# Performance work log

Hardware: AMD Instinct MI355X
Metric: run time of the kernel (lower is better)

The kernel has to match this reference:

```python
import jax, jax.numpy as jnp
import numpy as np

D = 1024      # model dim
DH = 64       # dim_head
H = 8         # heads
INNER = DH * H
L = 6         # depth
NL = 64       # num_latents
MF = 128      # max_num_frames
FF = 4 * D    # ff_mult * dim
B, T, F, V = 4, 8, 4, 256


def _ln(x, g, b):
    m = x.mean(-1, keepdims=True)
    v = x.var(-1, keepdims=True)
    return (x - m) / jnp.sqrt(v + 1e-5) * g + b


def setup_inputs() -> dict:
    key = jax.random.key(0)
    ks = jax.random.split(key, 8)
    s = 0.02
    x = jax.random.normal(ks[0], (B, T, F, V, D), jnp.float32)
    latents = jax.random.normal(ks[1], (NL, D), jnp.float32)
    frame_embs = jax.random.normal(ks[2], (MF, D), jnp.float32)
    Wq = jax.random.normal(ks[3], (L, D, INNER), jnp.float32) * s
    Wkv = jax.random.normal(ks[4], (L, D, 2 * INNER), jnp.float32) * s
    Wo = jax.random.normal(ks[5], (L, INNER, D), jnp.float32) * s
    W1 = jax.random.normal(ks[6], (L, D, FF), jnp.float32) * s
    W2 = jax.random.normal(ks[7], (L, FF, D), jnp.float32) * s
    ones = jnp.ones((L, D), jnp.float32)
    zeros = jnp.zeros((L, D), jnp.float32)
    return dict(
        x=x, latents=latents, frame_embs=frame_embs,
        g_media=ones, b_media=zeros, g_lat=ones, b_lat=zeros,
        Wq=Wq, Wkv=Wkv, Wo=Wo, g_ff=ones, b_ff=zeros, W1=W1, W2=W2,
        g_out=jnp.ones((D,), jnp.float32), b_out=jnp.zeros((D,), jnp.float32),
    )


def reference(x, latents, frame_embs, g_media, b_media, g_lat, b_lat,
              Wq, Wkv, Wo, g_ff, b_ff, W1, W2, g_out, b_out):
    scale = DH ** -0.5
    # add frame embeddings (indexed by T, as in original code), merge F,v dims
    x = x + frame_embs[:T][None, :, None, None, :]
    x = x.reshape(B, T, F * V, D)
    lat0 = jnp.broadcast_to(latents, (B, T, NL, D))

    def split_heads(a):  # (b, t, n, h*d) -> (b, h, t, n, d)
        return a.reshape(B, T, -1, H, DH).transpose(0, 3, 1, 2, 4)

    def block(lat, p):
        gm, bm, gl, bl, wq, wkv, wo, gf, bf, w1, w2 = p
        xm = _ln(x, gm, bm)
        ln_l = _ln(lat, gl, bl)
        q = (ln_l @ wq) * scale
        kv = jnp.concatenate([xm, ln_l], axis=-2) @ wkv
        k, v = jnp.split(kv, 2, axis=-1)
        q, k, v = split_heads(q), split_heads(k), split_heads(v)
        sim = jnp.einsum('bhtid,bhtjd->bhtij', q, k)
        attn = jax.nn.softmax(sim, axis=-1)
        o = jnp.einsum('bhtij,bhtjd->bhtid', attn, v)
        o = o.transpose(0, 2, 3, 1, 4).reshape(B, T, NL, INNER)
        lat = o @ wo + lat
        ff = jax.nn.gelu(_ln(lat, gf, bf) @ w1, approximate=False) @ w2
        return lat + ff, None

    lat, _ = jax.lax.scan(block, lat0,
                          (g_media, b_media, g_lat, b_lat, Wq, Wkv, Wo,
                           g_ff, b_ff, W1, W2))
    return _ln(lat, g_out, b_out)
```

## Files before the change

### kernel.cpp

```cpp
#include <hip/hip_runtime.h>
#include <math.h>

#define D_      1024
#define DH_     64
#define H_      8
#define INNER_  512
#define L_      6
#define NL_     64
#define FF_     4096
#define B_      4
#define T_      8
#define FV_     1024
#define BT_     32
#define MROWS_  32768
#define NKV_    1088
#define KVROWS_ 34816
#define ZB_     256

typedef __bf16 bf16;
typedef __bf16 bf16x8 __attribute__((ext_vector_type(8)));
typedef __bf16 bf16x4 __attribute__((ext_vector_type(4)));
typedef float  f32x4  __attribute__((ext_vector_type(4)));

#define BARRIER() { asm volatile("" ::: "memory"); __builtin_amdgcn_s_barrier(); asm volatile("" ::: "memory"); }
#define ENDPH() { __builtin_amdgcn_sched_barrier(0); asm volatile("s_waitcnt lgkmcnt(0)"); __builtin_amdgcn_sched_barrier(0); BARRIER(); }

__device__ __forceinline__ void gload_lds16(const bf16* g, bf16* l) {
    __builtin_amdgcn_global_load_lds(
        (const __attribute__((address_space(1))) unsigned int*)g,
        (__attribute__((address_space(3))) unsigned int*)l, 16, 0, 0);
}

__device__ __forceinline__ float wred_sum(float v) {
#pragma unroll
    for (int o = 32; o > 0; o >>= 1) v += __shfl_xor(v, o, 64);
    return v;
}

__device__ __forceinline__ float gelu_f(float x) {
    return 0.5f * x * (1.0f + erff(x * 0.70710678118654752440f));
}

__global__ __launch_bounds__(256) void xhat_k(const float* __restrict__ x,
                                              const float* __restrict__ fe,
                                              bf16* __restrict__ xhat) {
    __shared__ float red[8];
    int row = blockIdx.x;
    int t = (row >> 10) & 7;
    const float* xr = x + (size_t)row * D_;
    const float* fr_ = fe + (size_t)t * D_;
    int tid = threadIdx.x, c = tid * 4;
    float4 v = *(const float4*)(xr + c);
    float4 f = *(const float4*)(fr_ + c);
    v.x += f.x; v.y += f.y; v.z += f.z; v.w += f.w;
    float s = v.x + v.y + v.z + v.w;
    float ss = v.x * v.x + v.y * v.y + v.z * v.z + v.w * v.w;
    s = wred_sum(s); ss = wred_sum(ss);
    if ((tid & 63) == 0) { red[tid >> 6] = s; red[4 + (tid >> 6)] = ss; }
    __syncthreads();
    s = red[0] + red[1] + red[2] + red[3];
    ss = red[4] + red[5] + red[6] + red[7];
    float mean = s * (1.0f / D_);
    float rstd = rsqrtf(ss * (1.0f / D_) - mean * mean + 1e-5f);
    bf16x4 o;
    o[0] = (bf16)((v.x - mean) * rstd);
    o[1] = (bf16)((v.y - mean) * rstd);
    o[2] = (bf16)((v.z - mean) * rstd);
    o[3] = (bf16)((v.w - mean) * rstd);
    *(bf16x4*)(xhat + (size_t)row * D_ + c) = o;
}

__global__ __launch_bounds__(256) void latinit_k(const float* __restrict__ latents,
                                                 float* __restrict__ lat) {
    int row = blockIdx.x;
    int i = row & 63;
    int c = threadIdx.x * 4;
    float4 v = *(const float4*)(latents + (size_t)i * D_ + c);
    *(float4*)(lat + (size_t)row * D_ + c) = v;
}

template<int OUTF>
__global__ __launch_bounds__(256) void ln_k(const float* __restrict__ in,
                                            const float* __restrict__ g,
                                            const float* __restrict__ b,
                                            void* __restrict__ out) {
    __shared__ float red[8];
    int row = blockIdx.x;
    const float* x = in + (size_t)row * D_;
    int tid = threadIdx.x, c = tid * 4;
    float4 v = *(const float4*)(x + c);
    float s = v.x + v.y + v.z + v.w;
    float ss = v.x * v.x + v.y * v.y + v.z * v.z + v.w * v.w;
    s = wred_sum(s); ss = wred_sum(ss);
    if ((tid & 63) == 0) { red[tid >> 6] = s; red[4 + (tid >> 6)] = ss; }
    __syncthreads();
    s = red[0] + red[1] + red[2] + red[3];
    ss = red[4] + red[5] + red[6] + red[7];
    float mean = s * (1.0f / D_);
    float rstd = rsqrtf(ss * (1.0f / D_) - mean * mean + 1e-5f);
    float4 gv = *(const float4*)(g + c);
    float4 bv = *(const float4*)(b + c);
    float o0 = (v.x - mean) * rstd * gv.x + bv.x;
    float o1 = (v.y - mean) * rstd * gv.y + bv.y;
    float o2 = (v.z - mean) * rstd * gv.z + bv.z;
    float o3 = (v.w - mean) * rstd * gv.w + bv.w;
    if (OUTF) {
        *(float4*)((float*)out + (size_t)row * D_ + c) = make_float4(o0, o1, o2, o3);
    } else {
        bf16x4 o; o[0] = (bf16)o0; o[1] = (bf16)o1; o[2] = (bf16)o2; o[3] = (bf16)o3;
        *(bf16x4*)((bf16*)out + (size_t)row * D_ + c) = o;
    }
}

template<int NP, int OUTF>
__global__ __launch_bounds__(256) void accln_k(float* __restrict__ lat,
                                               const float* __restrict__ p, long long s,
                                               const float* __restrict__ g,
                                               const float* __restrict__ b,
                                               void* __restrict__ out) {
    __shared__ float red[8];
    int row = blockIdx.x;
    int tid = threadIdx.x, c = tid * 4;
    float* lr = lat + (size_t)row * D_;
    float4 a = *(const float4*)(lr + c);
#pragma unroll
    for (int w = 0; w < NP; w++) {
        float4 x = *(const float4*)(p + (size_t)w * s + (size_t)row * D_ + c);
        a.x += x.x; a.y += x.y; a.z += x.z; a.w += x.w;
    }
    if (!OUTF) *(float4*)(lr + c) = a;
    float sm = a.x + a.y + a.z + a.w;
    float ss = a.x * a.x + a.y * a.y + a.z * a.z + a.w * a.w;
    sm = wred_sum(sm); ss = wred_sum(ss);
    if ((tid & 63) == 0) { red[tid >> 6] = sm; red[4 + (tid >> 6)] = ss; }
    __syncthreads();
    sm = red[0] + red[1] + red[2] + red[3];
    ss = red[4] + red[5] + red[6] + red[7];
    float mean = sm * (1.0f / D_);
    float rstd = rsqrtf(ss * (1.0f / D_) - mean * mean + 1e-5f);
    float4 gv = *(const float4*)(g + c);
    float4 bv = *(const float4*)(b + c);
    float o0 = (a.x - mean) * rstd * gv.x + bv.x;
    float o1 = (a.y - mean) * rstd * gv.y + bv.y;
    float o2 = (a.z - mean) * rstd * gv.z + bv.z;
    float o3 = (a.w - mean) * rstd * gv.w + bv.w;
    if (OUTF) {
        *(float4*)((float*)out + (size_t)row * D_ + c) = make_float4(o0, o1, o2, o3);
    } else {
        bf16x4 o; o[0] = (bf16)o0; o[1] = (bf16)o1; o[2] = (bf16)o2; o[3] = (bf16)o3;
        *(bf16x4*)((bf16*)out + (size_t)row * D_ + c) = o;
    }
}

__device__ __forceinline__ void wt_tile(const float* __restrict__ in, int R, int C,
                                        bf16* __restrict__ out, int bx, int by,
                                        const float* __restrict__ sc,
                                        const float* __restrict__ bm,
                                        float* __restrict__ bkv) {
    __shared__ float t[32][33];
    int c0 = bx * 32, r0 = by * 32;
    int tx = threadIdx.x & 31, ty = threadIdx.x >> 5;
#pragma unroll
    for (int i = 0; i < 4; i++)
        t[ty + i * 8][tx] = in[(size_t)(r0 + ty + i * 8) * C + c0 + tx];
    __syncthreads();
    float scale = sc ? sc[r0 + tx] : 1.0f;
#pragma unroll
    for (int i = 0; i < 4; i++)
        out[(size_t)(c0 + ty + i * 8) * R + r0 + tx] = (bf16)(t[tx][ty + i * 8] * scale);
    if (bm && ty == 0) {
        float s = 0.0f;
#pragma unroll
        for (int r = 0; r < 32; r++) s += bm[r0 + r] * t[r][tx];
        atomicAdd(&bkv[c0 + tx], s);
    }
}

__global__ __launch_bounds__(256) void wprep_k(const float* __restrict__ wq,
                                               const float* __restrict__ wkv,
                                               const float* __restrict__ wo,
                                               const float* __restrict__ w1,
                                               const float* __restrict__ w2,
                                               const float* __restrict__ gm,
                                               const float* __restrict__ bm,
                                               float* __restrict__ bkv,
                                               bf16* __restrict__ BcatQ,
                                               bf16* __restrict__ BcatKV,
                                               bf16* __restrict__ WkvTg,
                                               bf16* __restrict__ WoT,
                                               bf16* __restrict__ W1T,
                                               bf16* __restrict__ W2T) {
    int id = blockIdx.x;
    if (id < 512)            wt_tile(wq, D_, INNER_, BcatQ, id & 15, id >> 4, nullptr, nullptr, nullptr);
    else if (id < 1536)  { int i = id - 512;  wt_tile(wkv, D_, 2 * INNER_, BcatKV, i & 31, i >> 5, nullptr, nullptr, nullptr); }
    else if (id < 2560)  { int i = id - 1536; wt_tile(wkv, D_, 2 * INNER_, WkvTg, i & 31, i >> 5, gm, bm, bkv); }
    else if (id < 3072)  { int i = id - 2560; wt_tile(wo, INNER_, D_, WoT, i & 31, i >> 5, nullptr, nullptr, nullptr); }
    else if (id < 7168)  { int i = id - 3072; wt_tile(w1, D_, FF_, W1T, i & 127, i >> 7, nullptr, nullptr, nullptr); }
    else                 { int i = id - 7168; wt_tile(w2, FF_, D_, W2T, i & 31, i >> 5, nullptr, nullptr, nullptr); }
}

__global__ __launch_bounds__(512, 1) void gemm_kv(const bf16* __restrict__ Ag,
                                                  const bf16* __restrict__ Bg,
                                                  bf16* __restrict__ KVb,
                                                  bf16* __restrict__ vt,
                                                  const float* __restrict__ bias) {
    __shared__ bf16 lds[2][32768];
    const int lda = D_, ldb = D_;
    const int tid = threadIdx.x;
    const int w = tid >> 6, lane = tid & 63;
    const int wm = w >> 2, wn = w & 3;
    const size_t m0 = (size_t)blockIdx.x * 256;
    const size_t n0 = (size_t)blockIdx.y * 256;
    const int nt = 16;

    const int p0 = (w * 2) * 64 + lane, p1 = p0 + 64;
    const int sr0 = p0 >> 3, sk0 = ((p0 & 7) ^ (sr0 & 7)) * 8;
    const int sr1 = p1 >> 3, sk1 = ((p1 & 7) ^ (sr1 & 7)) * 8;
    const int scw0 = (w * 2) * 512, scw1 = scw0 + 512;

    auto STAGE = [&](const bf16* g, int ld, size_t row0, int k0, bf16* bufb, int rb) {
        gload_lds16(g + (row0 + sr0) * (size_t)ld + k0 + sk0, bufb + rb + scw0);
        gload_lds16(g + (row0 + sr1) * (size_t)ld + k0 + sk1, bufb + rb + scw1);
    };

    const int fr = lane & 15;
    const int pK0 = (((lane >> 4)) ^ (fr & 7)) * 8;
    const int pK1 = ((4 + (lane >> 4)) ^ (fr & 7)) * 8;
    const size_t aoff = (size_t)(wm * 128 + fr) * 64;
    const size_t boff = 16384 + (size_t)(wn * 64 + fr) * 64;

    f32x4 acc[8][4];
#pragma unroll
    for (int i = 0; i < 8; i++)
#pragma unroll
        for (int j = 0; j < 4; j++)
#pragma unroll
            for (int r = 0; r < 4; r++) acc[i][j][r] = 0.0f;

    STAGE(Bg, ldb, n0,       0, lds[0], 16384);
    STAGE(Bg, ldb, n0 + 128, 0, lds[0], 24576);
    STAGE(Ag, lda, m0,       0, lds[0], 0);
    STAGE(Ag, lda, m0 + 128, 0, lds[0], 8192);
    STAGE(Bg, ldb, n0,       64, lds[1], 16384);
    STAGE(Bg, ldb, n0 + 128, 64, lds[1], 24576);
    STAGE(Ag, lda, m0,       64, lds[1], 0);
    asm volatile("s_waitcnt vmcnt(6)");
    BARRIER();

    for (int t = 0; t < nt; ++t) {
        const bf16* lb = lds[t & 1];
        bf16* lbw = lds[t & 1];
        bf16* lbn = lds[(t + 1) & 1];
        const int kt1 = (t + 1) << 6, kt2 = (t + 2) << 6;
        bf16x8 bfr[4][2];

        {
#pragma unroll
            for (int j = 0; j < 4; j++) {
                bfr[j][0] = *(const bf16x8*)(lb + boff + j * 1024 + pK0);
                bfr[j][1] = *(const bf16x8*)(lb + boff + j * 1024 + pK1);
            }
            bf16x8 a00 = *(const bf16x8*)(lb + aoff + 0 * 1024 + pK0);
            bf16x8 a01 = *(const bf16x8*)(lb + aoff + 0 * 1024 + pK1);
            bf16x8 a10 = *(const bf16x8*)(lb + aoff + 1 * 1024 + pK0);
            bf16x8 a11 = *(const bf16x8*)(lb + aoff + 1 * 1024 + pK1);
            if (t + 1 < nt) STAGE(Ag, lda, m0 + 128, kt1, lbn, 8192);
            BARRIER();
            asm volatile("s_waitcnt lgkmcnt(0)");
            __builtin_amdgcn_s_setprio(1);
#pragma unroll
            for (int j = 0; j < 4; j++) {
                acc[0][j] = __builtin_amdgcn_mfma_f32_16x16x32_bf16(a00, bfr[j][0], acc[0][j], 0, 0, 0);
                acc[0][j] = __builtin_amdgcn_mfma_f32_16x16x32_bf16(a01, bfr[j][1], acc[0][j], 0, 0, 0);
                acc[1][j] = __builtin_amdgcn_mfma_f32_16x16x32_bf16(a10, bfr[j][0], acc[1][j], 0, 0, 0);
                acc[1][j] = __builtin_amdgcn_mfma_f32_16x16x32_bf16(a11, bfr[j][1], acc[1][j], 0, 0, 0);
            }
            __builtin_amdgcn_s_setprio(0);
            BARRIER();
        }
        {
            bf16x8 a00 = *(const bf16x8*)(lb + aoff + 2 * 1024 + pK0);
            bf16x8 a01 = *(const bf16x8*)(lb + aoff + 2 * 1024 + pK1);
            bf16x8 a10 = *(const bf16x8*)(lb + aoff + 3 * 1024 + pK0);
            bf16x8 a11 = *(const bf16x8*)(lb + aoff + 3 * 1024 + pK1);
            if (t + 2 < nt) STAGE(Bg, ldb, n0, kt2, lbw, 16384);
            BARRIER();
            asm volatile("s_waitcnt lgkmcnt(0)");
            __builtin_amdgcn_s_setprio(1);
#pragma unroll
            for (int j = 0; j < 4; j++) {
                acc[2][j] = __builtin_amdgcn_mfma_f32_16x16x32_bf16(a00, bfr[j][0], acc[2][j], 0, 0, 0);
                acc[2][j] = __builtin_amdgcn_mfma_f32_16x16x32_bf16(a01, bfr[j][1], acc[2][j], 0, 0, 0);
                acc[3][j] = __builtin_amdgcn_mfma_f32_16x16x32_bf16(a10, bfr[j][0], acc[3][j], 0, 0, 0);
                acc[3][j] = __builtin_amdgcn_mfma_f32_16x16x32_bf16(a11, bfr[j][1], acc[3][j], 0, 0, 0);
            }
            __builtin_amdgcn_s_setprio(0);
            BARRIER();
        }
        {
            bf16x8 a00 = *(const bf16x8*)(lb + aoff + 4 * 1024 + pK0);
            bf16x8 a01 = *(const bf16x8*)(lb + aoff + 4 * 1024 + pK1);
            bf16x8 a10 = *(const bf16x8*)(lb + aoff + 5 * 1024 + pK0);
            bf16x8 a11 = *(const bf16x8*)(lb + aoff + 5 * 1024 + pK1);
            if (t + 2 < nt) STAGE(Bg, ldb, n0 + 128, kt2, lbw, 24576);
            BARRIER();
            asm volatile("s_waitcnt lgkmcnt(0)");
            __builtin_amdgcn_s_setprio(1);
#pragma unroll
            for (int j = 0; j < 4; j++) {
                acc[4][j] = __builtin_amdgcn_mfma_f32_16x16x32_bf16(a00, bfr[j][0], acc[4][j], 0, 0, 0);
                acc[4][j] = __builtin_amdgcn_mfma_f32_16x16x32_bf16(a01, bfr[j][1], acc[4][j], 0, 0, 0);
                acc[5][j] = __builtin_amdgcn_mfma_f32_16x16x32_bf16(a10, bfr[j][0], acc[5][j], 0, 0, 0);
                acc[5][j] = __builtin_amdgcn_mfma_f32_16x16x32_bf16(a11, bfr[j][1], acc[5][j], 0, 0, 0);
            }
            __builtin_amdgcn_s_setprio(0);
            BARRIER();
        }
        {
            bf16x8 a00 = *(const bf16x8*)(lb + aoff + 6 * 1024 + pK0);
            bf16x8 a01 = *(const bf16x8*)(lb + aoff + 6 * 1024 + pK1);
            bf16x8 a10 = *(const bf16x8*)(lb + aoff + 7 * 1024 + pK0);
            bf16x8 a11 = *(const bf16x8*)(lb + aoff + 7 * 1024 + pK1);
            if (t + 2 < nt) STAGE(Ag, lda, m0, kt2, lbw, 0);
            BARRIER();
            asm volatile("s_waitcnt lgkmcnt(0)");
            __builtin_amdgcn_s_setprio(1);
#pragma unroll
            for (int j = 0; j < 4; j++) {
                acc[6][j] = __builtin_amdgcn_mfma_f32_16x16x32_bf16(a00, bfr[j][0], acc[6][j], 0, 0, 0);
                acc[6][j] = __builtin_amdgcn_mfma_f32_16x16x32_bf16(a01, bfr[j][1], acc[6][j], 0, 0, 0);
                acc[7][j] = __builtin_amdgcn_mfma_f32_16x16x32_bf16(a10, bfr[j][0], acc[7][j], 0, 0, 0);
                acc[7][j] = __builtin_amdgcn_mfma_f32_16x16x32_bf16(a11, bfr[j][1], acc[7][j], 0, 0, 0);
            }
            __builtin_amdgcn_s_setprio(0);
            if (t < nt - 2)       { asm volatile("s_waitcnt vmcnt(6)"); }
            else if (t == nt - 2) { asm volatile("s_waitcnt vmcnt(0)"); }
            BARRIER();
        }
    }

    const int fq = (lane >> 4) * 4;
#pragma unroll
    for (int i = 0; i < 8; i++)
#pragma unroll
        for (int j = 0; j < 4; j++) {
            size_t cb = n0 + wn * 64 + j * 16 + fr;
            float bv = bias[cb];
            size_t mb = m0 + wm * 128 + i * 16 + fq;
            if (cb < 512) {
#pragma unroll
                for (int r = 0; r < 4; r++) {
                    size_t m = mb + r;
                    size_t rb = m + ((m >> 10) << 6);
                    KVb[rb * 512 + cb] = (bf16)(acc[i][j][r] + bv);
                }
            } else {
                int hh = ((int)cb - 512) >> 6, dh = ((int)cb - 512) & 63;
                size_t bt = mb >> 10, jl = mb & 1023;
                bf16x4 v4;
#pragma unroll
                for (int r = 0; r < 4; r++) v4[r] = (bf16)(acc[i][j][r] + bv);
                *(bf16x4*)(vt + ((bt * 8 + hh) * 64 + dh) * (size_t)NKV_ + jl) = v4;
            }
        }
}

template<int MODE>
__global__ __launch_bounds__(512, 1) void gemm_ff(const bf16* __restrict__ Ag, int lda,
                                                  const bf16* __restrict__ Bg, int ldb,
                                                  void* __restrict__ C, int ldc,
                                                  int K, long long czs) {
    __shared__ bf16 lds[2][24576];
    const int tid = threadIdx.x;
    const int w = tid >> 6, lane = tid & 63;
    const int wm = w >> 2, wn = w & 3;
    const size_t m0 = (size_t)blockIdx.x * 128;
    const size_t n0 = (size_t)blockIdx.y * 256;
    const int klen = K / gridDim.z;
    const int koff = blockIdx.z * klen;
    const int nt = klen >> 6;

    const int p0 = (w * 2) * 64 + lane, p1 = p0 + 64;
    const int sr0 = p0 >> 3, sk0 = ((p0 & 7) ^ (sr0 & 7)) * 8;
    const int sr1 = p1 >> 3, sk1 = ((p1 & 7) ^ (sr1 & 7)) * 8;
    const int scw0 = (w * 2) * 512, scw1 = scw0 + 512;

    auto STAGE = [&](const bf16* g, int ld, size_t row0, int k0, bf16* bufb, int rb) {
        gload_lds16(g + (row0 + sr0) * (size_t)ld + k0 + sk0, bufb + rb + scw0);
        gload_lds16(g + (row0 + sr1) * (size_t)ld + k0 + sk1, bufb + rb + scw1);
    };

    const int fr = lane & 15;
    const int pK0 = (((lane >> 4)) ^ (fr & 7)) * 8;
    const int pK1 = ((4 + (lane >> 4)) ^ (fr & 7)) * 8;
    const size_t aoff = (size_t)(wm * 64 + fr) * 64;
    const size_t boff = 8192 + (size_t)(wn * 64 + fr) * 64;

    f32x4 acc[4][4];
#pragma unroll
    for (int i = 0; i < 4; i++)
#pragma unroll
        for (int j = 0; j < 4; j++)
#pragma unroll
            for (int r = 0; r < 4; r++) acc[i][j][r] = 0.0f;

    bf16x8 aX[2], aY[2], bA[4][2], bB[4][2];

    auto LDA1 = [&](const bf16* lb, int i0, bf16x8 (&d)[2]) {
        d[0] = *(const bf16x8*)(lb + aoff + (size_t)i0 * 1024 + pK0);
        d[1] = *(const bf16x8*)(lb + aoff + (size_t)i0 * 1024 + pK1);
    };
    auto LDB8 = [&](const bf16* lb, bf16x8 (&bb)[4][2]) {
#pragma unroll
        for (int j = 0; j < 4; j++) {
            bb[j][0] = *(const bf16x8*)(lb + boff + j * 1024 + pK0);
            bb[j][1] = *(const bf16x8*)(lb + boff + j * 1024 + pK1);
        }
    };
    auto MM1 = [&](int i0, bf16x8 (&a)[2], bf16x8 (&bb)[4][2]) {
        __builtin_amdgcn_s_setprio(1);
#pragma unroll
        for (int j = 0; j < 4; j++) {
            acc[i0][j] = __builtin_amdgcn_mfma_f32_16x16x32_bf16(a[0], bb[j][0], acc[i0][j], 0, 0, 0);
            acc[i0][j] = __builtin_amdgcn_mfma_f32_16x16x32_bf16(a[1], bb[j][1], acc[i0][j], 0, 0, 0);
        }
        __builtin_amdgcn_s_setprio(0);
    };

    STAGE(Ag, lda, m0,       koff,      lds[0], 0);
    STAGE(Bg, ldb, n0,       koff,      lds[0], 8192);
    STAGE(Bg, ldb, n0 + 128, koff,      lds[0], 16384);
    STAGE(Bg, ldb, n0,       koff + 64, lds[1], 8192);
    STAGE(Bg, ldb, n0 + 128, koff + 64, lds[1], 16384);
    asm volatile("s_waitcnt vmcnt(4)");
    BARRIER();
    LDB8(lds[0], bA);
    LDA1(lds[0], 0, aX);

    auto tile4 = [&](const bf16* lb, bf16* lbn, bf16x8 (&BU)[4][2], bf16x8 (&BL)[4][2], int t) {
        bf16* lbw = (bf16*)lb;
        LDA1(lb, 1, aY);
        if (t + 1 < nt) STAGE(Ag, lda, m0, koff + ((t + 1) << 6), lbn, 0);
        MM1(0, aX, BU);
        ENDPH();
        LDA1(lb, 2, aX);
        if (t + 2 < nt) STAGE(Bg, ldb, n0, koff + ((t + 2) << 6), lbw, 8192);
        MM1(1, aY, BU);
        ENDPH();
        LDA1(lb, 3, aY);
        if (t + 2 < nt) STAGE(Bg, ldb, n0 + 128, koff + ((t + 2) << 6), lbw, 16384);
        MM1(2, aX, BU);
        __builtin_amdgcn_sched_barrier(0);
        asm volatile("s_waitcnt lgkmcnt(0)");
        __builtin_amdgcn_sched_barrier(0);
        if (t < nt - 2)       { asm volatile("s_waitcnt vmcnt(4)"); }
        else if (t == nt - 2) { asm volatile("s_waitcnt vmcnt(0)"); }
        BARRIER();
        if (t + 1 < nt) { LDB8(lbn, BL); LDA1(lbn, 0, aX); }
        MM1(3, aY, BU);
        ENDPH();
    };

    for (int t = 0; t < nt; t += 2) {
        tile4(lds[0], lds[1], bA, bB, t);
        tile4(lds[1], lds[0], bB, bA, t + 1);
    }

    const int fq = (lane >> 4) * 4;
#pragma unroll
    for (int i = 0; i < 4; i++)
#pragma unroll
        for (int j = 0; j < 4; j++) {
            size_t cb = n0 + wn * 64 + j * 16 + fr;
            size_t mb = m0 + wm * 64 + i * 16 + fq;
#pragma unroll
            for (int r = 0; r < 4; r++) {
                float v = acc[i][j][r];
                if (MODE == 4) {
                    ((float*)C + blockIdx.z * czs)[(mb + r) * (size_t)ldc + cb] = v;
                } else {
                    ((bf16*)C)[(mb + r) * (size_t)ldc + cb] = (bf16)gelu_f(v);
                }
            }
        }
}

template<int MODE, int CMAP>
__global__ __launch_bounds__(256) void gemm128(const bf16* __restrict__ A, int lda,
                                               const bf16* __restrict__ Bw, int ldb,
                                               void* __restrict__ C, int ldc,
                                               int K, float scale,
                                               long long czs, void* __restrict__ C2,
                                               void* __restrict__ C3) {
    __shared__ bf16 As[128 * 32];
    __shared__ bf16 Bs[128 * 32];
    const int tid = threadIdx.x;
    const int wave = tid >> 6;
    const int lane = tid & 63;
    const size_t m0 = (size_t)blockIdx.x * 128;
    const size_t n0 = (size_t)blockIdx.y * 128;
    const int wm = (wave >> 1) * 64;
    const int wn = (wave & 1) * 64;

    const int klen = K / gridDim.z;
    const int koff = blockIdx.z * klen;

    const int r0 = tid >> 2;
    const int c0 = ((tid & 3) ^ ((tid >> 3) & 3)) * 8;
    const bf16* ga0 = A + (m0 + r0) * lda + c0 + koff;
    const bf16* ga1 = A + (m0 + r0 + 64) * lda + c0 + koff;
    const bf16* gb0 = Bw + (n0 + r0) * ldb + c0 + koff;
    const bf16* gb1 = Bw + (n0 + r0 + 64) * ldb + c0 + koff;
    bf16* la0 = As + wave * 512;
    bf16* la1 = As + 2048 + wave * 512;
    bf16* lb0 = Bs + wave * 512;
    bf16* lb1 = Bs + 2048 + wave * 512;

    f32x4 acc[4][4];
#pragma unroll
    for (int i = 0; i < 4; i++)
#pragma unroll
        for (int j = 0; j < 4; j++)
#pragma unroll
            for (int r = 0; r < 4; r++) acc[i][j][r] = 0.0f;

    const int fr = lane & 15;
    const int q = lane >> 4;
    const int sw = (q ^ ((fr >> 1) & 3)) * 8;

    for (int kt = 0; kt < klen; kt += 32) {
        gload_lds16(ga0 + kt, la0);
        gload_lds16(ga1 + kt, la1);
        gload_lds16(gb0 + kt, lb0);
        gload_lds16(gb1 + kt, lb1);
        __syncthreads();
        bf16x8 af[4], bfv[4];
#pragma unroll
        for (int i = 0; i < 4; i++) {
            af[i]  = *(const bf16x8*)(As + (wm + i * 16 + fr) * 32 + sw);
            bfv[i] = *(const bf16x8*)(Bs + (wn + i * 16 + fr) * 32 + sw);
        }
#pragma unroll
        for (int i = 0; i < 4; i++)
#pragma unroll
            for (int j = 0; j < 4; j++)
                acc[i][j] = __builtin_amdgcn_mfma_f32_16x16x32_bf16(af[i], bfv[j], acc[i][j], 0, 0, 0);
        __syncthreads();
    }

    const int fq = (lane >> 4) * 4;
#pragma unroll
    for (int i = 0; i < 4; i++)
#pragma unroll
        for (int j = 0; j < 4; j++) {
            size_t cb = n0 + wn + j * 16 + fr;
            size_t mb = m0 + wm + i * 16 + fq;
            if (CMAP == 3) {
                if (cb < 512) {
#pragma unroll
                    for (int r = 0; r < 4; r++)
                        ((bf16*)C)[(mb + r) * 512 + cb] = (bf16)(acc[i][j][r] * scale);
                } else if (cb < 1024) {
#pragma unroll
                    for (int r = 0; r < 4; r++) {
                        size_t m = mb + r;
                        size_t rb = (m >> 6) * (size_t)NKV_ + 1024 + (m & 63);
                        ((bf16*)C2)[rb * 512 + (cb - 512)] = (bf16)acc[i][j][r];
                    }
                } else {
                    int hh = ((int)cb - 1024) >> 6, dh = ((int)cb - 1024) & 63;
                    size_t bt = mb >> 6, jl = 1024 + (mb & 63);
                    bf16x4 v4;
#pragma unroll
                    for (int r = 0; r < 4; r++) v4[r] = (bf16)acc[i][j][r];
                    *(bf16x4*)((bf16*)C3 + ((bt * 8 + hh) * 64 + dh) * (size_t)NKV_ + jl) = v4;
                }
            } else {
#pragma unroll
                for (int r = 0; r < 4; r++) {
                    float v = acc[i][j][r];
                    if (MODE == 4) {
                        ((float*)C + blockIdx.z * czs)[(mb + r) * ldc + cb] = v;
                    } else {
                        ((bf16*)C)[(mb + r) * ldc + cb] = (bf16)v;
                    }
                }
            }
        }
}

__global__ __launch_bounds__(256, 2) void attn_k(const bf16* __restrict__ qb,
                                                 const bf16* __restrict__ KVb,
                                                 const bf16* __restrict__ vt,
                                                 bf16* __restrict__ ob) {
    __shared__ float comb[4][64 * 66];
    __shared__ float sc[4][64];
    __shared__ float mw[4][64], lw[4][64];
    const int z = blockIdx.x, bt = z >> 3, h = z & 7;
    const int tid = threadIdx.x, w = tid >> 6, lane = tid & 63;
    const int fr = lane & 15, g = lane >> 4;
    const bf16* Qz = qb + (size_t)(bt * 64) * INNER_ + h * DH_;
    const bf16* Kz = KVb + (size_t)bt * NKV_ * 512 + h * DH_;
    const bf16* Vz = vt + (size_t)z * (DH_ * NKV_);
    bf16* Pw = (bf16*)(&comb[w][0]);

    bf16x8 qf[4][2];
#pragma unroll
    for (int nj = 0; nj < 4; nj++)
#pragma unroll
        for (int ks = 0; ks < 2; ks++)
            qf[nj][ks] = *(const bf16x8*)(Qz + (size_t)(fr + 16 * nj) * INNER_ + g * 8 + ks * 32);

    f32x4 acc_o[4][4];
#pragma unroll
    for (int i = 0; i < 4; i++)
#pragma unroll
        for (int j = 0; j < 4; j++)
#pragma unroll
            for (int r = 0; r < 4; r++) acc_o[i][j][r] = 0.0f;
    float m_reg[4] = {-INFINITY, -INFINITY, -INFINITY, -INFINITY};
    float l_reg[4] = {0.0f, 0.0f, 0.0f, 0.0f};

    const int nch = (w == 0) ? 5 : 4;
    for (int ci = 0; ci < nch; ci++) {
        const int kc0 = (w + ci * 4) * 64;
        f32x4 s[4][4];
#pragma unroll
        for (int i = 0; i < 4; i++)
#pragma unroll
            for (int j = 0; j < 4; j++)
#pragma unroll
                for (int r = 0; r < 4; r++) s[i][j][r] = 0.0f;
#pragma unroll
        for (int ks = 0; ks < 2; ks++) {
            bf16x8 kf[4];
#pragma unroll
            for (int mi = 0; mi < 4; mi++)
                kf[mi] = *(const bf16x8*)(Kz + (size_t)(kc0 + fr + 16 * mi) * 512 + g * 8 + ks * 32);
#pragma unroll
            for (int mi = 0; mi < 4; mi++)
#pragma unroll
                for (int nj = 0; nj < 4; nj++)
                    s[mi][nj] = __builtin_amdgcn_mfma_f32_16x16x32_bf16(kf[mi], qf[nj][ks], s[mi][nj], 0, 0, 0);
        }
        float pmax[4];
#pragma unroll
        for (int nj = 0; nj < 4; nj++) {
            float mx = s[0][nj][0];
#pragma unroll
            for (int mi = 0; mi < 4; mi++)
#pragma unroll
                for (int r = 0; r < 4; r++) mx = fmaxf(mx, s[mi][nj][r]);
            mx = fmaxf(mx, __shfl_xor(mx, 16, 64));
            mx = fmaxf(mx, __shfl_xor(mx, 32, 64));
            pmax[nj] = mx;
        }
        bool grew = (pmax[0] > m_reg[0]) || (pmax[1] > m_reg[1]) ||
                    (pmax[2] > m_reg[2]) || (pmax[3] > m_reg[3]);
        if (__any(grew ? 1 : 0)) {
            float so[4];
#pragma unroll
            for (int nj = 0; nj < 4; nj++) {
                float mn = fmaxf(m_reg[nj], pmax[nj]);
                so[nj] = __expf(m_reg[nj] - mn);
                m_reg[nj] = mn;
                l_reg[nj] *= so[nj];
            }
            if (g == 0) {
#pragma unroll
                for (int nj = 0; nj < 4; nj++) sc[w][fr + 16 * nj] = so[nj];
            }
            asm volatile("s_waitcnt lgkmcnt(0)" ::: "memory");
#pragma unroll
            for (int mi = 0; mi < 4; mi++)
#pragma unroll
                for (int r = 0; r < 4; r++) {
                    float sq = sc[w][16 * mi + 4 * g + r];
#pragma unroll
                    for (int jd = 0; jd < 4; jd++) acc_o[mi][jd][r] *= sq;
                }
        }
        float psum[4] = {0.0f, 0.0f, 0.0f, 0.0f};
#pragma unroll
        for (int mi = 0; mi < 4; mi++)
#pragma unroll
            for (int nj = 0; nj < 4; nj++) {
                bf16x4 pb4;
#pragma unroll
                for (int r = 0; r < 4; r++) {
                    float pv = __expf(s[mi][nj][r] - m_reg[nj]);
                    psum[nj] += pv;
                    pb4[r] = (bf16)pv;
                }
                *(bf16x4*)(Pw + (size_t)(fr + 16 * nj) * 72 + 16 * mi + 4 * g) = pb4;
            }
#pragma unroll
        for (int nj = 0; nj < 4; nj++) {
            float ps = psum[nj];
            ps += __shfl_xor(ps, 16, 64);
            ps += __shfl_xor(ps, 32, 64);
            l_reg[nj] += ps;
        }
        asm volatile("s_waitcnt lgkmcnt(0)" ::: "memory");
#pragma unroll
        for (int ks = 0; ks < 2; ks++) {
            bf16x8 af[4], vf[4];
#pragma unroll
            for (int mi = 0; mi < 4; mi++)
                af[mi] = *(const bf16x8*)(Pw + (size_t)(fr + 16 * mi) * 72 + g * 8 + ks * 32);
#pragma unroll
            for (int jd = 0; jd < 4; jd++)
                vf[jd] = *(const bf16x8*)(Vz + (size_t)(fr + 16 * jd) * NKV_ + kc0 + g * 8 + ks * 32);
#pragma unroll
            for (int mi = 0; mi < 4; mi++)
#pragma unroll
                for (int jd = 0; jd < 4; jd++)
                    acc_o[mi][jd] = __builtin_amdgcn_mfma_f32_16x16x32_bf16(af[mi], vf[jd], acc_o[mi][jd], 0, 0, 0);
        }
    }

    if (g == 0) {
#pragma unroll
        for (int nj = 0; nj < 4; nj++) {
            mw[w][fr + 16 * nj] = m_reg[nj];
            lw[w][fr + 16 * nj] = l_reg[nj];
        }
    }
    asm volatile("s_waitcnt lgkmcnt(0)" ::: "memory");
#pragma unroll
    for (int mi = 0; mi < 4; mi++)
#pragma unroll
        for (int jd = 0; jd < 4; jd++)
#pragma unroll
            for (int r = 0; r < 4; r++)
                comb[w][(16 * mi + 4 * g + r) * 66 + fr + 16 * jd] = acc_o[mi][jd][r];
    __syncthreads();
    {
        int q = tid >> 2, d0 = (tid & 3) * 16;
        float M = fmaxf(fmaxf(mw[0][q], mw[1][q]), fmaxf(mw[2][q], mw[3][q]));
        float al[4], l = 0.0f;
#pragma unroll
        for (int ww = 0; ww < 4; ww++) { al[ww] = __expf(mw[ww][q] - M); l += al[ww] * lw[ww][q]; }
        float inv = 1.0f / l;
        bf16 outv[16];
#pragma unroll
        for (int dd = 0; dd < 16; dd++) {
            float o = 0.0f;
#pragma unroll
            for (int ww = 0; ww < 4; ww++) o += comb[ww][q * 66 + d0 + dd] * al[ww];
            outv[dd] = (bf16)(o * inv);
        }
        bf16* dst = ob + (size_t)(bt * 64 + q) * INNER_ + h * 64 + d0;
        *(bf16x8*)dst = *(bf16x8*)outv;
        *(bf16x8*)(dst + 8) = *(bf16x8*)(outv + 8);
    }
}

extern "C" void kernel_launch(void* const* d_in, const int* in_sizes, int n_in,
                              void* d_out, int out_size, void* d_ws, size_t ws_size,
                              hipStream_t stream) {
    const float* x       = (const float*)d_in[0];
    const float* latents = (const float*)d_in[1];
    const float* fe      = (const float*)d_in[2];
    const float* g_media = (const float*)d_in[3];
    const float* b_media = (const float*)d_in[4];
    const float* g_lat   = (const float*)d_in[5];
    const float* b_lat   = (const float*)d_in[6];
    const float* Wq      = (const float*)d_in[7];
    const float* Wkv     = (const float*)d_in[8];
    const float* Wo      = (const float*)d_in[9];
    const float* g_ff    = (const float*)d_in[10];
    const float* b_ff    = (const float*)d_in[11];
    const float* W1      = (const float*)d_in[12];
    const float* W2      = (const float*)d_in[13];
    const float* g_out   = (const float*)d_in[14];
    const float* b_out   = (const float*)d_in[15];

    char* p = (char*)d_ws;
    auto alloc = [&](size_t bytes) { char* r = p; p += (bytes + 255) & ~(size_t)255; return r; };
    bf16*  xhat = (bf16*)alloc((size_t)MROWS_ * D_ * 2);
    float* lat  = (float*)alloc((size_t)2048 * D_ * 4);
    bf16*  lnl  = (bf16*)alloc((size_t)2048 * D_ * 2);
    bf16*  qb   = (bf16*)alloc((size_t)2048 * INNER_ * 2);
    bf16*  KVb  = (bf16*)alloc((size_t)KVROWS_ * 512 * 2);
    bf16*  vt   = (bf16*)alloc((size_t)ZB_ * DH_ * NKV_ * 2);
    bf16*  ob   = (bf16*)alloc((size_t)2048 * INNER_ * 2);
    bf16*  Bcat = (bf16*)alloc((size_t)1536 * D_ * 2);
    bf16*  WkvTg= (bf16*)alloc((size_t)D_ * D_ * 2);
    bf16*  WoT  = (bf16*)alloc((size_t)D_ * INNER_ * 2);
    bf16*  W1T  = (bf16*)alloc((size_t)FF_ * D_ * 2);
    bf16*  W2T  = (bf16*)alloc((size_t)D_ * FF_ * 2);
    float* bkv  = (float*)alloc(1024 * 4);
    float* ffp  = (float*)alloc((size_t)4 * 2048 * D_ * 4);
    bf16*  ffh  = vt;

    xhat_k<<<MROWS_, 256, 0, stream>>>(x, fe, xhat);
    latinit_k<<<2048, 256, 0, stream>>>(latents, lat);
    ln_k<0><<<2048, 256, 0, stream>>>(lat, g_lat, b_lat, lnl);

    const long long PS = (long long)2048 * D_;

    for (int l = 0; l < L_; l++) {
        const float* gm = g_media + (size_t)l * D_;
        const float* bm = b_media + (size_t)l * D_;
        const float* gf = g_ff + (size_t)l * D_;
        const float* bf_ = b_ff + (size_t)l * D_;
        const float* wq = Wq + (size_t)l * D_ * INNER_;
        const float* wkv = Wkv + (size_t)l * D_ * 2 * INNER_;
        const float* wo = Wo + (size_t)l * INNER_ * D_;
        const float* w1 = W1 + (size_t)l * D_ * FF_;
        const float* w2 = W2 + (size_t)l * FF_ * D_;

        hipMemsetAsync(bkv, 0, 1024 * 4, stream);
        wprep_k<<<11264, 256, 0, stream>>>(wq, wkv, wo, w1, w2, gm, bm, bkv,
                                           Bcat, Bcat + (size_t)512 * D_, WkvTg, WoT, W1T, W2T);

        gemm_kv<<<dim3(128, 4), 512, 0, stream>>>(xhat, WkvTg, KVb, vt, bkv);
        gemm128<0, 3><<<dim3(16, 12), 256, 0, stream>>>(
            lnl, D_, Bcat, D_, qb, 0, D_, 0.125f, 0, KVb, vt);

        attn_k<<<ZB_, 256, 0, stream>>>(qb, KVb, vt, ob);

        gemm128<4, 0><<<dim3(16, 8, 2), 256, 0, stream>>>(
            ob, INNER_, WoT, INNER_, ffp, D_, INNER_, 1.0f, PS, nullptr, nullptr);
        accln_k<2, 0><<<2048, 256, 0, stream>>>(lat, ffp, PS, gf, bf_, lnl);

        gemm_ff<3><<<dim3(16, 16), 512, 0, stream>>>(
            lnl, D_, W1T, D_, ffh, FF_, D_, 0);
        gemm_ff<4><<<dim3(16, 4, 4), 512, 0, stream>>>(
            ffh, FF_, W2T, FF_, ffp, D_, FF_, PS);
        if (l < L_ - 1) {
            accln_k<4, 0><<<2048, 256, 0, stream>>>(lat, ffp, PS,
                g_lat + (size_t)(l + 1) * D_, b_lat + (size_t)(l + 1) * D_, lnl);
        } else {
            accln_k<4, 1><<<2048, 256, 0, stream>>>(lat, ffp, PS, g_out, b_out, (float*)d_out);
        }
    }
}
```

Before: 1.280 ms.

## Batch weight prep for all layers and split attention KV across two blocks

Weight transposition and bf16 conversion for all six layers now runs in one up-front launch instead of one launch plus a memset per layer, which cuts per-layer launch overhead at the cost of larger workspace buffers. Attention splits each (bt,head) KV range into two halves handled by separate blocks, doubling the grid from 256 to 512 blocks for better CU occupancy. A new combine kernel merges the two partials using their max and sum statistics, adding an extra launch and fp32 partial traffic. The online-softmax rescale now fires only when the running max grows by more than 8, skipping some rescale work in exchange for a looser bound on exponent range.

```diff
diff --git a/kernel.cpp b/kernel.cpp
--- a/kernel.cpp
+++ b/kernel.cpp
@@ -176,21 +176,35 @@
     }
 }
 
-__global__ __launch_bounds__(256) void wprep_k(const float* __restrict__ wq,
-                                               const float* __restrict__ wkv,
-                                               const float* __restrict__ wo,
-                                               const float* __restrict__ w1,
-                                               const float* __restrict__ w2,
-                                               const float* __restrict__ gm,
-                                               const float* __restrict__ bm,
-                                               float* __restrict__ bkv,
-                                               bf16* __restrict__ BcatQ,
-                                               bf16* __restrict__ BcatKV,
-                                               bf16* __restrict__ WkvTg,
-                                               bf16* __restrict__ WoT,
-                                               bf16* __restrict__ W1T,
-                                               bf16* __restrict__ W2T) {
-    int id = blockIdx.x;
+__global__ __launch_bounds__(256) void wprep_all(const float* __restrict__ Wq,
+                                                 const float* __restrict__ Wkv,
+                                                 const float* __restrict__ Wo,
+                                                 const float* __restrict__ W1,
+                                                 const float* __restrict__ W2,
+                                                 const float* __restrict__ g_media,
+                                                 const float* __restrict__ b_media,
+                                                 float* __restrict__ bkv6,
+                                                 bf16* __restrict__ Bcat6,
+                                                 bf16* __restrict__ WkvTg6,
+                                                 bf16* __restrict__ WoT6,
+                                                 bf16* __restrict__ W1T6,
+                                                 bf16* __restrict__ W2T6) {
+    int l = blockIdx.x / 11264;
+    int id = blockIdx.x - l * 11264;
+    const float* wq  = Wq + (size_t)l * D_ * INNER_;
+    const float* wkv = Wkv + (size_t)l * D_ * 2 * INNER_;
+    const float* wo  = Wo + (size_t)l * INNER_ * D_;
+    const float* w1  = W1 + (size_t)l * D_ * FF_;
+    const float* w2  = W2 + (size_t)l * FF_ * D_;
+    bf16* BcatQ  = Bcat6 + (size_t)l * 1536 * D_;
+    bf16* BcatKV = BcatQ + (size_t)512 * D_;
+    bf16* WkvTg  = WkvTg6 + (size_t)l * D_ * D_;
+    bf16* WoT    = WoT6 + (size_t)l * D_ * INNER_;
+    bf16* W1T    = W1T6 + (size_t)l * FF_ * D_;
+    bf16* W2T    = W2T6 + (size_t)l * D_ * FF_;
+    const float* gm = g_media + (size_t)l * D_;
+    const float* bm = b_media + (size_t)l * D_;
+    float* bkv = bkv6 + (size_t)l * 1024;
     if (id < 512)            wt_tile(wq, D_, INNER_, BcatQ, id & 15, id >> 4, nullptr, nullptr, nullptr);
     else if (id < 1536)  { int i = id - 512;  wt_tile(wkv, D_, 2 * INNER_, BcatKV, i & 31, i >> 5, nullptr, nullptr, nullptr); }
     else if (id < 2560)  { int i = id - 1536; wt_tile(wkv, D_, 2 * INNER_, WkvTg, i & 31, i >> 5, gm, bm, bkv); }
@@ -592,11 +606,14 @@
 __global__ __launch_bounds__(256, 2) void attn_k(const bf16* __restrict__ qb,
                                                  const bf16* __restrict__ KVb,
                                                  const bf16* __restrict__ vt,
-                                                 bf16* __restrict__ ob) {
+                                                 float* __restrict__ partO,
+                                                 float* __restrict__ partML) {
     __shared__ float comb[4][64 * 66];
     __shared__ float sc[4][64];
     __shared__ float mw[4][64], lw[4][64];
-    const int z = blockIdx.x, bt = z >> 3, h = z & 7;
+    const int bid = blockIdx.x;
+    const int z = bid >> 1, half = bid & 1;
+    const int bt = z >> 3, h = z & 7;
     const int tid = threadIdx.x, w = tid >> 6, lane = tid & 63;
     const int fr = lane & 15, g = lane >> 4;
     const bf16* Qz = qb + (size_t)(bt * 64) * INNER_ + h * DH_;
@@ -621,9 +638,10 @@
     float m_reg[4] = {-INFINITY, -INFINITY, -INFINITY, -INFINITY};
     float l_reg[4] = {0.0f, 0.0f, 0.0f, 0.0f};
 
-    const int nch = (w == 0) ? 5 : 4;
+    const int cbase = half ? 9 : 0;
+    const int nch = half ? 2 : ((w == 0) ? 3 : 2);
     for (int ci = 0; ci < nch; ci++) {
-        const int kc0 = (w + ci * 4) * 64;
+        const int kc0 = (cbase + w + ci * 4) * 64;
         f32x4 s[4][4];
 #pragma unroll
         for (int i = 0; i < 4; i++)
@@ -655,9 +673,9 @@
             mx = fmaxf(mx, __shfl_xor(mx, 32, 64));
             pmax[nj] = mx;
         }
-        bool grew = (pmax[0] > m_reg[0]) || (pmax[1] > m_reg[1]) ||
-                    (pmax[2] > m_reg[2]) || (pmax[3] > m_reg[3]);
-        if (__any(grew ? 1 : 0)) {
+        bool big = (pmax[0] > m_reg[0] + 8.0f) || (pmax[1] > m_reg[1] + 8.0f) ||
+                   (pmax[2] > m_reg[2] + 8.0f) || (pmax[3] > m_reg[3] + 8.0f);
+        if (__any(big ? 1 : 0)) {
             float so[4];
 #pragma unroll
             for (int nj = 0; nj < 4; nj++) {
@@ -741,19 +759,41 @@
         float al[4], l = 0.0f;
 #pragma unroll
         for (int ww = 0; ww < 4; ww++) { al[ww] = __expf(mw[ww][q] - M); l += al[ww] * lw[ww][q]; }
-        float inv = 1.0f / l;
-        bf16 outv[16];
+        float* pO = partO + (size_t)bid * 4096 + q * 64 + d0;
 #pragma unroll
         for (int dd = 0; dd < 16; dd++) {
             float o = 0.0f;
 #pragma unroll
             for (int ww = 0; ww < 4; ww++) o += comb[ww][q * 66 + d0 + dd] * al[ww];
-            outv[dd] = (bf16)(o * inv);
-        }
-        bf16* dst = ob + (size_t)(bt * 64 + q) * INNER_ + h * 64 + d0;
-        *(bf16x8*)dst = *(bf16x8*)outv;
-        *(bf16x8*)(dst + 8) = *(bf16x8*)(outv + 8);
-    }
+            pO[dd] = o;
+        }
+        if ((tid & 3) == 0) {
+            partML[bid * 128 + q] = M;
+            partML[bid * 128 + 64 + q] = l;
+        }
+    }
+}
+
+__global__ __launch_bounds__(256) void attn_comb(const float* __restrict__ partO,
+                                                 const float* __restrict__ partML,
+                                                 bf16* __restrict__ ob) {
+    int z = blockIdx.x, bt = z >> 3, h = z & 7;
+    int tid = threadIdx.x, q = tid >> 2, d0 = (tid & 3) * 16;
+    int b0 = z * 2, b1 = z * 2 + 1;
+    float M0 = partML[b0 * 128 + q], l0 = partML[b0 * 128 + 64 + q];
+    float M1 = partML[b1 * 128 + q], l1 = partML[b1 * 128 + 64 + q];
+    float M = fmaxf(M0, M1);
+    float a0 = __expf(M0 - M), a1 = __expf(M1 - M);
+    float inv = 1.0f / (a0 * l0 + a1 * l1);
+    const float* pO0 = partO + (size_t)b0 * 4096 + q * 64 + d0;
+    const float* pO1 = partO + (size_t)b1 * 4096 + q * 64 + d0;
+    bf16 outv[16];
+#pragma unroll
+    for (int dd = 0; dd < 16; dd++)
+        outv[dd] = (bf16)((a0 * pO0[dd] + a1 * pO1[dd]) * inv);
+    bf16* dst = ob + (size_t)(bt * 64 + q) * INNER_ + h * 64 + d0;
+    *(bf16x8*)dst = *(bf16x8*)outv;
+    *(bf16x8*)(dst + 8) = *(bf16x8*)(outv + 8);
 }
 
 extern "C" void kernel_launch(void* const* d_in, const int* in_sizes, int n_in,
@@ -778,48 +818,49 @@
 
     char* p = (char*)d_ws;
     auto alloc = [&](size_t bytes) { char* r = p; p += (bytes + 255) & ~(size_t)255; return r; };
-    bf16*  xhat = (bf16*)alloc((size_t)MROWS_ * D_ * 2);
-    float* lat  = (float*)alloc((size_t)2048 * D_ * 4);
-    bf16*  lnl  = (bf16*)alloc((size_t)2048 * D_ * 2);
-    bf16*  qb   = (bf16*)alloc((size_t)2048 * INNER_ * 2);
-    bf16*  KVb  = (bf16*)alloc((size_t)KVROWS_ * 512 * 2);
-    bf16*  vt   = (bf16*)alloc((size_t)ZB_ * DH_ * NKV_ * 2);
-    bf16*  ob   = (bf16*)alloc((size_t)2048 * INNER_ * 2);
-    bf16*  Bcat = (bf16*)alloc((size_t)1536 * D_ * 2);
-    bf16*  WkvTg= (bf16*)alloc((size_t)D_ * D_ * 2);
-    bf16*  WoT  = (bf16*)alloc((size_t)D_ * INNER_ * 2);
-    bf16*  W1T  = (bf16*)alloc((size_t)FF_ * D_ * 2);
-    bf16*  W2T  = (bf16*)alloc((size_t)D_ * FF_ * 2);
-    float* bkv  = (float*)alloc(1024 * 4);
-    float* ffp  = (float*)alloc((size_t)4 * 2048 * D_ * 4);
-    bf16*  ffh  = vt;
+    bf16*  xhat  = (bf16*)alloc((size_t)MROWS_ * D_ * 2);
+    float* lat   = (float*)alloc((size_t)2048 * D_ * 4);
+    bf16*  lnl   = (bf16*)alloc((size_t)2048 * D_ * 2);
+    bf16*  qb    = (bf16*)alloc((size_t)2048 * INNER_ * 2);
+    bf16*  KVb   = (bf16*)alloc((size_t)KVROWS_ * 512 * 2);
+    bf16*  vt    = (bf16*)alloc((size_t)ZB_ * DH_ * NKV_ * 2);
+    bf16*  ob    = (bf16*)alloc((size_t)2048 * INNER_ * 2);
+    bf16*  Bcat6 = (bf16*)alloc((size_t)L_ * 1536 * D_ * 2);
+    bf16*  WkvTg6= (bf16*)alloc((size_t)L_ * D_ * D_ * 2);
+    bf16*  WoT6  = (bf16*)alloc((size_t)L_ * D_ * INNER_ * 2);
+    bf16*  W1T6  = (bf16*)alloc((size_t)L_ * FF_ * D_ * 2);
+    bf16*  W2T6  = (bf16*)alloc((size_t)L_ * D_ * FF_ * 2);
+    float* bkv6  = (float*)alloc((size_t)L_ * 1024 * 4);
+    float* ffp   = (float*)alloc((size_t)4 * 2048 * D_ * 4);
+    bf16*  ffh   = vt;
+    float* partO = ffp;
+    float* partML= ffp + (size_t)512 * 4096;
 
     xhat_k<<<MROWS_, 256, 0, stream>>>(x, fe, xhat);
     latinit_k<<<2048, 256, 0, stream>>>(latents, lat);
     ln_k<0><<<2048, 256, 0, stream>>>(lat, g_lat, b_lat, lnl);
+    hipMemsetAsync(bkv6, 0, (size_t)L_ * 1024 * 4, stream);
+    wprep_all<<<L_ * 11264, 256, 0, stream>>>(Wq, Wkv, Wo, W1, W2, g_media, b_media,
+                                              bkv6, Bcat6, WkvTg6, WoT6, W1T6, W2T6);
 
     const long long PS = (long long)2048 * D_;
 
     for (int l = 0; l < L_; l++) {
-        const float* gm = g_media + (size_t)l * D_;
-        const float* bm = b_media + (size_t)l * D_;
         const float* gf = g_ff + (size_t)l * D_;
         const float* bf_ = b_ff + (size_t)l * D_;
-        const float* wq = Wq + (size_t)l * D_ * INNER_;
-        const float* wkv = Wkv + (size_t)l * D_ * 2 * INNER_;
-        const float* wo = Wo + (size_t)l * INNER_ * D_;
-        const float* w1 = W1 + (size_t)l * D_ * FF_;
-        const float* w2 = W2 + (size_t)l * FF_ * D_;
-
-        hipMemsetAsync(bkv, 0, 1024 * 4, stream);
-        wprep_k<<<11264, 256, 0, stream>>>(wq, wkv, wo, w1, w2, gm, bm, bkv,
-                                           Bcat, Bcat + (size_t)512 * D_, WkvTg, WoT, W1T, W2T);
+        bf16* Bcat  = Bcat6 + (size_t)l * 1536 * D_;
+        bf16* WkvTg = WkvTg6 + (size_t)l * D_ * D_;
+        bf16* WoT   = WoT6 + (size_t)l * D_ * INNER_;
+        bf16* W1T   = W1T6 + (size_t)l * FF_ * D_;
+        bf16* W2T   = W2T6 + (size_t)l * D_ * FF_;
+        float* bkv  = bkv6 + (size_t)l * 1024;
 
         gemm_kv<<<dim3(128, 4), 512, 0, stream>>>(xhat, WkvTg, KVb, vt, bkv);
         gemm128<0, 3><<<dim3(16, 12), 256, 0, stream>>>(
             lnl, D_, Bcat, D_, qb, 0, D_, 0.125f, 0, KVb, vt);
 
-        attn_k<<<ZB_, 256, 0, stream>>>(qb, KVb, vt, ob);
+        attn_k<<<2 * ZB_, 256, 0, stream>>>(qb, KVb, vt, partO, partML);
+        attn_comb<<<ZB_, 256, 0, stream>>>(partO, partML, ob);
 
         gemm128<4, 0><<<dim3(16, 8, 2), 256, 0, stream>>>(
             ob, INNER_, WoT, INNER_, ffp, D_, INNER_, 1.0f, PS, nullptr, nullptr);
```

New measurement: 1.330 ms. 3.9% more time.
